# Optimization experiments

Measured on AMD Instinct MI355X. Metric: run time of the kernel, lower is better.

## Reference

```python
import jax, jax.numpy as jnp
import numpy as np

B, S, D, H = 2, 2048, 1024, 16
DH = D // H  # d_head = 64
EPS = 1e-6


def _rms_norm(x, eps=EPS):
    # norm_without_weight: RMS normalization over last dim, no learned scale
    return x * jax.lax.rsqrt(jnp.mean(x * x, axis=-1, keepdims=True) + eps)


def _rope_tables(seq_len, dim):
    # angular_freq: dim//4 geometric freqs + dim//4 zeros -> dim//2 total
    freqs = (1.0 / 1024.0) ** jnp.linspace(0.0, 1.0, dim // 4, dtype=jnp.float32)
    freqs = jnp.concatenate([freqs, jnp.zeros((dim // 4,), dtype=jnp.float32)])
    theta = jnp.outer(jnp.arange(seq_len, dtype=jnp.float32), freqs)  # [S, dim//2]
    return jnp.cos(theta), jnp.sin(theta)


def _apply_rope(x_bhsk, cos, sin):
    # x: [B,H,S,DH]; cos/sin: [S, DH//2] broadcast over batch/heads
    c = cos[None, None, :, :]
    s = sin[None, None, :, :]
    xf = x_bhsk.astype(jnp.float32)
    x1, x2 = jnp.split(xf, 2, axis=-1)
    y1 = x1 * c + x2 * s
    y2 = -x1 * s + x2 * c
    return jnp.concatenate([y1, y2], axis=-1).astype(x_bhsk.dtype)


def setup_inputs() -> dict:
    key = jax.random.key(0)
    k0, k1, k2, k3, k4 = jax.random.split(key, 5)
    scale = 1.0 / np.sqrt(D)
    x = jax.random.normal(k0, (B, S, D), dtype=jnp.float32)
    # equinox Linear stores weight as [out_features, in_features], y = x @ W.T
    w_q = jax.random.normal(k1, (D, D), dtype=jnp.float32) * scale
    w_k = jax.random.normal(k2, (D, D), dtype=jnp.float32) * scale
    w_v = jax.random.normal(k3, (D, D), dtype=jnp.float32) * scale
    w_o = jax.random.normal(k4, (D, D), dtype=jnp.float32) * scale
    mask = jnp.tril(jnp.ones((S, S), dtype=bool))  # causal
    return {"x": x, "w_q": w_q, "w_k": w_k, "w_v": w_v, "w_o": w_o, "mask": mask}


def reference(x, w_q, w_k, w_v, w_o, mask):
    b, s, d = x.shape
    # projections (no bias); [B,S,D] @ [D,D].T -> [B,S,D] -> [B,H,S,DH]
    def proj(w):
        y = jnp.einsum('bsd,ed->bse', x, w)
        return y.reshape(b, s, H, DH).transpose(0, 2, 1, 3)
    q, k, v = proj(w_q), proj(w_k), proj(w_v)
    # QK-norm (RMS, no weight)
    q = _rms_norm(q)
    k = _rms_norm(k)
    # rotary over sequence axis
    cos, sin = _rope_tables(s, DH)
    q = _apply_rope(q, cos, sin)
    k = _apply_rope(k, cos, sin)
    # scores [B,H,S,S]
    scores = jnp.einsum('bhsk,bhtk->bhst', q, k) / jnp.sqrt(jnp.float32(DH))
    scores = jnp.where(mask[None, None, :, :], scores, -jnp.inf)
    weights = jax.nn.softmax(scores, axis=-1)
    out = jnp.einsum('bhst,bhtk->bhsk', weights, v)  # [B,H,S,DH]
    out = out.transpose(0, 2, 1, 3).reshape(b, s, d)
    return jnp.einsum('bsd,ed->bse', out, w_o)
```

## Files before the change

kernel.cpp:

```cpp
#include <hip/hip_runtime.h>
#include <hip/hip_bf16.h>

#define Bb 2
#define Ss 2048
#define Dd 1024
#define Hh 16
#define Tt ((size_t)Bb*Ss*Dd)
#define WNn ((size_t)Dd*Dd)

typedef short bf16x8 __attribute__((ext_vector_type(8)));
typedef short bf16x4 __attribute__((ext_vector_type(4)));
typedef float floatx4 __attribute__((ext_vector_type(4)));
typedef unsigned short u16;

__device__ inline void gld16(void* lds, const void* g) {
  __builtin_amdgcn_global_load_lds(
      (const __attribute__((address_space(1))) unsigned int*)g,
      (__attribute__((address_space(3))) unsigned int*)lds, 16, 0, 0);
}

__device__ inline float bf2f(u16 u) {
  unsigned int x = ((unsigned int)u) << 16;
  float f; __builtin_memcpy(&f, &x, 4); return f;
}
__device__ inline u16 f2bf(float f) {
  unsigned int x; __builtin_memcpy(&x, &f, 4);
  x = (x + 0x7fff + ((x >> 16) & 1)) >> 16;
  return (u16)x;
}
__device__ inline float u2f(unsigned int x) {
  float f; __builtin_memcpy(&f, &x, 4); return f;
}
__device__ inline unsigned int cvtpk(float lo, float hi) {
  unsigned int r;
  asm("v_cvt_pk_bf16_f32 %0, %1, %2" : "=v"(r) : "v"(lo), "v"(hi));
  return r;
}

__global__ void sniff(const unsigned int* __restrict__ x, unsigned int* __restrict__ flag,
                      int nwords) {
  __shared__ int cnt;
  if (threadIdx.x == 0) cnt = 0;
  __syncthreads();
  int local = 0;
  for (int i = threadIdx.x; i < nwords; i += blockDim.x) {
    unsigned int wd = x[i];
    if (((wd >> 7)  & 0xFFu) == 0xFFu) local++;
    if (((wd >> 23) & 0xFFu) == 0xFFu) local++;
  }
  atomicAdd(&cnt, local);
  __syncthreads();
  if (threadIdx.x == 0) *flag = (cnt >= 64) ? 1u : 0u;
}

__global__ __launch_bounds__(256) void convert_all(
    const void* __restrict__ x,  const void* __restrict__ wq,
    const void* __restrict__ wk, const void* __restrict__ wv,
    const void* __restrict__ wo, u16* __restrict__ dst,
    int smode, const unsigned int* __restrict__ flag,
    float2* __restrict__ tab) {
  const int gb = blockIdx.x;
  if (gb >= 4096) {
    int e = (gb - 4096)*1024 + threadIdx.x*4;
#pragma unroll
    for (int j = 0; j < 4; j++, e++) {
      int s = e >> 4, f = e & 15;
      float freq = exp2f((-10.0f/15.0f) * (float)f);
      float th = (float)s * freq;
      float sn, c;
      sincosf(th, &sn, &c);
      tab[e] = make_float2(c, sn);
    }
    return;
  }
  const void* src; size_t base; int lb;
  if (gb < 2048)      { src = x;  base = 0;            lb = gb;        }
  else if (gb < 2560) { src = wq; base = Tt;           lb = gb - 2048; }
  else if (gb < 3072) { src = wk; base = Tt + WNn;     lb = gb - 2560; }
  else if (gb < 3584) { src = wv; base = Tt + 2*WNn;   lb = gb - 3072; }
  else                { src = wo; base = Tt + 3*WNn;   lb = gb - 3584; }
  const size_t off = (size_t)lb*2048 + threadIdx.x*8;
  const bool f32 = (smode >= 0) ? (smode == 1) : (*flag != 0u);
  bf16x8 v;
  if (f32) {
    const float* s = (const float*)src + off;
#pragma unroll
    for (int j = 0; j < 8; j++) v[j] = (short)f2bf(s[j]);
  } else {
    v = *(const bf16x8*)((const u16*)src + off);
  }
  *(bf16x8*)(dst + base + off) = v;
}

__global__ __launch_bounds__(256) void gemm_bt(
    const u16* __restrict__ A,
    const u16* __restrict__ W0, const u16* __restrict__ W1, const u16* __restrict__ W2,
    void* __restrict__ C0, void* __restrict__ C1, void* __restrict__ C2,
    int M, int N, int K, const unsigned int* __restrict__ flag, int outMode, int mode,
    const float2* __restrict__ tab)
{
  const u16* W; void* C;
  if (blockIdx.z == 0)      { W = W0; C = C0; }
  else if (blockIdx.z == 1) { W = W1; C = C1; }
  else                      { W = W2; C = C2; }

  __shared__ __align__(16) u16 sA[128*32];
  __shared__ __align__(16) u16 sB[128*32];

  const int tid  = threadIdx.x;
  const int lane = tid & 63;
  const int w    = tid >> 6;
  const int wm = w >> 1, wn = w & 1;
  const int col = lane & 15, quad = lane >> 4;
  const int bm = blockIdx.y, bn = blockIdx.x;

  floatx4 acc[4][4] = {};

  const int c0 = tid, c1 = tid + 256;
  const size_t aOff0 = (size_t)(bm*128 + (c0 >> 2))*K + (c0 & 3)*8;
  const size_t aOff1 = (size_t)(bm*128 + (c1 >> 2))*K + (c1 & 3)*8;
  const size_t bOff0 = (size_t)(bn*128 + (c0 >> 2))*K + (c0 & 3)*8;
  const size_t bOff1 = (size_t)(bn*128 + (c1 >> 2))*K + (c1 & 3)*8;

  for (int kk = 0; kk < K; kk += 32) {
    gld16(&sA[c0*8], A + aOff0 + kk);
    gld16(&sA[c1*8], A + aOff1 + kk);
    gld16(&sB[c0*8], W + bOff0 + kk);
    gld16(&sB[c1*8], W + bOff1 + kk);
    __syncthreads();
    bf16x8 af[4], bfr[4];
#pragma unroll
    for (int i = 0; i < 4; i++)
      af[i] = *(const bf16x8*)&sA[(wm*64 + i*16 + col)*32 + quad*8];
#pragma unroll
    for (int j = 0; j < 4; j++)
      bfr[j] = *(const bf16x8*)&sB[(wn*64 + j*16 + col)*32 + quad*8];
#pragma unroll
    for (int i = 0; i < 4; i++)
#pragma unroll
      for (int j = 0; j < 4; j++)
        acc[i][j] = __builtin_amdgcn_mfma_f32_16x16x32_bf16(af[i], bfr[j], acc[i][j], 0, 0, 0);
    __syncthreads();
  }

  if (mode == 0 && blockIdx.z == 2) {
    u16* Ct = (u16*)C;
#pragma unroll
    for (int i = 0; i < 4; i++)
#pragma unroll
      for (int j = 0; j < 4; j++) {
        int d = bn*128 + wn*64 + j*16 + col;
        int g = bm*128 + wm*64 + i*16 + quad*4;
        int hh = d >> 6, dl = d & 63;
        int bb = g >> 11, s = g & (Ss - 1);
        bf16x4 pk;
#pragma unroll
        for (int r = 0; r < 4; r++) pk[r] = (short)f2bf(acc[i][j][r]);
        *(bf16x4*)&Ct[((size_t)(bb*Hh + hh)*64 + dl)*Ss + s] = pk;
      }
  } else if (mode == 0) {
    const float qs = (blockIdx.z == 0) ? 0.125f : 1.0f;
    u16* Co = (u16*)C;
    const size_t cb = (size_t)(bn*128 + wn*64 + col);
#pragma unroll
    for (int i = 0; i < 4; i++)
#pragma unroll
      for (int r = 0; r < 4; r++) {
        float ss = 0.0f;
#pragma unroll
        for (int j = 0; j < 4; j++) ss += acc[i][j][r]*acc[i][j][r];
        ss += __shfl_xor(ss, 1, 64);
        ss += __shfl_xor(ss, 2, 64);
        ss += __shfl_xor(ss, 4, 64);
        ss += __shfl_xor(ss, 8, 64);
        float rn = rsqrtf(ss*(1.0f/64.0f) + 1e-6f) * qs;
        int grow = bm*128 + wm*64 + i*16 + quad*4 + r;
        float2 cs = tab[(grow & (Ss - 1))*16 + col];
        float c = cs.x, sn = cs.y;
        float x0 = acc[i][0][r]*rn, x1 = acc[i][1][r]*rn;
        float x2 = acc[i][2][r]*rn, x3 = acc[i][3][r]*rn;
        size_t rowb = (size_t)grow*N + cb;
        Co[rowb]      = f2bf(x0*c + x2*sn);
        Co[rowb + 16] = f2bf(x1);
        Co[rowb + 32] = f2bf(x2*c - x0*sn);
        Co[rowb + 48] = f2bf(x3);
      }
  } else {
    const bool f32o = (outMode == 1) || (outMode == -1 && *flag != 0u);
#pragma unroll
    for (int i = 0; i < 4; i++)
#pragma unroll
      for (int j = 0; j < 4; j++)
#pragma unroll
        for (int r = 0; r < 4; r++) {
          int grow = bm*128 + wm*64 + i*16 + quad*4 + r;
          int gcol = bn*128 + wn*64 + j*16 + col;
          size_t idx = (size_t)grow*N + gcol;
          float v = acc[i][j][r];
          if (f32o) ((float*)C)[idx] = v;
          else      ((u16*)C)[idx]   = f2bf(v);
        }
  }
}

__global__ __launch_bounds__(256) void attn(
    const u16* __restrict__ Q, const u16* __restrict__ Kv,
    const u16* __restrict__ Vt, u16* __restrict__ O)
{
  __shared__ __align__(16) u16 sK[2][64*72];
  __shared__ __align__(16) u16 sV[2][2][64*32];
  __shared__ __align__(16) u16 sP[4][16*72];

  const int tid  = threadIdx.x;
  const int lane = tid & 63;
  const int w    = tid >> 6;
  const int col = lane & 15, quad = lane >> 4;
  const int bh = blockIdx.x;
  const int qt = 31 - (int)blockIdx.y;
  const int b = bh >> 4, h = bh & 15;
  const size_t base  = (size_t)b*Ss*Dd + (size_t)h*64;
  const size_t vbase = (size_t)bh*64*Ss;

  const int krow = tid >> 2;
  const int kch  = (tid & 3) * 2;
  const int vrow = tid >> 2;
  const int vcp  = (tid & 3) ^ (vrow & 3) ^ ((vrow >> 2) & 3);
  const u16* Vh = Vt + vbase + (size_t)vrow*Ss + vcp*8;
  const int xorv = quad ^ (col & 3) ^ ((col >> 2) & 3);
  u16* sPw = &sP[w][0];
  const float L2E = 1.44269504f;

  const int q0 = qt * 64;
  const int nk = qt + 1;
  const int qmin = q0 + w*16;

  bf16x8 qf0, qf1;
  {
    const size_t qoff = base + (size_t)(q0 + w*16 + col)*Dd + quad*8;
    qf0 = *(const bf16x8*)(Q + qoff);
    qf1 = *(const bf16x8*)(Q + qoff + 32);
  }
  floatx4 oacc[4] = {};
  float mi[4], li[4];
#pragma unroll
  for (int r = 0; r < 4; r++) { mi[r] = -1e30f; li[r] = 0.0f; }

  {
    const u16* kg = Kv + base + (size_t)krow*Dd + kch*8;
    bf16x8 ka = *(const bf16x8*)kg;
    bf16x8 kb = *(const bf16x8*)(kg + 8);
    gld16(&sV[0][0][tid*8], Vh);
    gld16(&sV[0][1][tid*8], Vh + 32);
    *(bf16x8*)&sK[0][krow*72 + kch*8]     = ka;
    *(bf16x8*)&sK[0][krow*72 + kch*8 + 8] = kb;
    __syncthreads();
  }

  for (int kt = 0; kt < nk; kt++) {
    const int t0 = kt*64;
    const int cur = kt & 1, nxt = cur ^ 1;
    const bool more = (kt + 1 < nk);
    bf16x8 ka, kb;
    if (more) {
      const u16* kg = Kv + base + (size_t)(t0 + 64 + krow)*Dd + kch*8;
      ka = *(const bf16x8*)kg;
      kb = *(const bf16x8*)(kg + 8);
      gld16(&sV[nxt][0][tid*8], Vh + t0 + 64);
      gld16(&sV[nxt][1][tid*8], Vh + t0 + 96);
    }

    floatx4 sc[4] = {};
    __builtin_amdgcn_s_setprio(1);
#pragma unroll
    for (int ts = 0; ts < 4; ts++) {
      bf16x8 k0 = *(const bf16x8*)&sK[cur][(ts*16 + col)*72 + quad*8];
      bf16x8 k1 = *(const bf16x8*)&sK[cur][(ts*16 + col)*72 + 32 + quad*8];
      sc[ts] = __builtin_amdgcn_mfma_f32_16x16x32_bf16(qf0, k0, sc[ts], 0,0,0);
      sc[ts] = __builtin_amdgcn_mfma_f32_16x16x32_bf16(qf1, k1, sc[ts], 0,0,0);
    }
    __builtin_amdgcn_s_setprio(0);

    const bool boundary = (t0 + 63 > qmin);
    float mxr[4];
    float needmax = 0.0f;
#pragma unroll
    for (int r = 0; r < 4; r++) {
      if (boundary) {
        const int qr = q0 + w*16 + quad*4 + r;
        if (t0 +      col > qr) sc[0][r] = -1e30f;
        if (t0 + 16 + col > qr) sc[1][r] = -1e30f;
        if (t0 + 32 + col > qr) sc[2][r] = -1e30f;
        if (t0 + 48 + col > qr) sc[3][r] = -1e30f;
      }
      float mx = fmaxf(fmaxf(sc[0][r], sc[1][r]), fmaxf(sc[2][r], sc[3][r]));
      mx = fmaxf(mx, __shfl_xor(mx, 1, 64));
      mx = fmaxf(mx, __shfl_xor(mx, 2, 64));
      mx = fmaxf(mx, __shfl_xor(mx, 4, 64));
      mx = fmaxf(mx, __shfl_xor(mx, 8, 64));
      mxr[r] = mx;
      needmax = fmaxf(needmax, mx - mi[r]);
    }
    if (!__all(needmax <= 8.0f)) {
      float alr[4];
#pragma unroll
      for (int r = 0; r < 4; r++) {
        float mn = fmaxf(mi[r], mxr[r]);
        float al = exp2f((mi[r] - mn)*L2E);
        mi[r] = mn; li[r] *= al; alr[r] = al;
      }
#pragma unroll
      for (int db = 0; db < 4; db++)
#pragma unroll
        for (int r = 0; r < 4; r++) oacc[db][r] *= alr[r];
    }
#pragma unroll
    for (int r = 0; r < 4; r++) {
      const float nb = -mi[r]*L2E;
      float p0 = exp2f(fmaf(sc[0][r], L2E, nb));
      float p1 = exp2f(fmaf(sc[1][r], L2E, nb));
      float p2 = exp2f(fmaf(sc[2][r], L2E, nb));
      float p3 = exp2f(fmaf(sc[3][r], L2E, nb));
      unsigned int pk01 = cvtpk(p0, p1);
      unsigned int pk23 = cvtpk(p2, p3);
      const int rw = (quad*4 + r)*72;
      sPw[rw + col]      = (u16)pk01;
      sPw[rw + 16 + col] = (u16)(pk01 >> 16);
      sPw[rw + 32 + col] = (u16)pk23;
      sPw[rw + 48 + col] = (u16)(pk23 >> 16);
      li[r] += (u2f(pk01 << 16) + u2f(pk01 & 0xffff0000u))
             + (u2f(pk23 << 16) + u2f(pk23 & 0xffff0000u));
    }
    bf16x8 pa0 = *(const bf16x8*)&sPw[col*72 + quad*8];
    bf16x8 pa1 = *(const bf16x8*)&sPw[col*72 + 32 + quad*8];
    __builtin_amdgcn_s_setprio(1);
#pragma unroll
    for (int db = 0; db < 4; db++) {
      const int vs = (db*16 + col)*32 + xorv*8;
      bf16x8 vb0 = *(const bf16x8*)&sV[cur][0][vs];
      bf16x8 vb1 = *(const bf16x8*)&sV[cur][1][vs];
      oacc[db] = __builtin_amdgcn_mfma_f32_16x16x32_bf16(pa0, vb0, oacc[db], 0,0,0);
      oacc[db] = __builtin_amdgcn_mfma_f32_16x16x32_bf16(pa1, vb1, oacc[db], 0,0,0);
    }
    __builtin_amdgcn_s_setprio(0);

    if (more) {
      *(bf16x8*)&sK[nxt][krow*72 + kch*8]     = ka;
      *(bf16x8*)&sK[nxt][krow*72 + kch*8 + 8] = kb;
    }
    __syncthreads();
  }

  float inv[4];
#pragma unroll
  for (int r = 0; r < 4; r++) {
    float s = li[r];
    s += __shfl_xor(s, 1, 64);
    s += __shfl_xor(s, 2, 64);
    s += __shfl_xor(s, 4, 64);
    s += __shfl_xor(s, 8, 64);
    inv[r] = 1.0f / s;
  }
#pragma unroll
  for (int db = 0; db < 4; db++)
#pragma unroll
    for (int r = 0; r < 4; r++)
      O[base + (size_t)(q0 + w*16 + quad*4 + r)*Dd + db*16 + col] =
          f2bf(oacc[db][r] * inv[r]);
}

extern "C" void kernel_launch(void* const* d_in, const int* in_sizes, int n_in,
                              void* d_out, int out_size, void* d_ws, size_t ws_size,
                              hipStream_t stream) {
  const void* x  = d_in[0];
  const void* wq = d_in[1];
  const void* wk = d_in[2];
  const void* wv = d_in[3];
  const void* wo = d_in[4];

  const size_t T  = Tt;
  const size_t WN = WNn;

  char* ws = (char*)d_ws;
  unsigned int* flag = (unsigned int*)ws;
  u16* xb  = (u16*)(ws + 256);
  u16* wqb = xb  + T;
  u16* wkb = wqb + WN;
  u16* wvb = wkb + WN;
  u16* wob = wvb + WN;
  u16* Qb  = wob + WN;
  u16* Kb  = Qb + T;
  u16* Vb  = Kb + T;
  u16* AO  = Vb + T;
  float2* tab = (float2*)(AO + T);

  int smode = -1;
  if (in_sizes && n_in > 0) {
    if (in_sizes[0] == (int)(T*4))      smode = 1;
    else if (in_sizes[0] == (int)(T*2)) smode = 0;
  }
  if (smode < 0)
    sniff<<<1, 1024, 0, stream>>>((const unsigned int*)x, flag, 65536);

  convert_all<<<4128, 256, 0, stream>>>(x, wq, wk, wv, wo, xb, smode, flag, tab);

  gemm_bt<<<dim3(8, 32, 3), 256, 0, stream>>>(xb, wqb, wkb, wvb, Qb, Kb, Vb,
                                              4096, 1024, 1024, flag, 0, 0, tab);
  attn<<<dim3(32, 32), 256, 0, stream>>>(Qb, Kb, Vb, AO);
  gemm_bt<<<dim3(8, 32, 1), 256, 0, stream>>>(AO, wob, wob, wob, d_out, d_out, d_out,
                                              4096, 1024, 1024, flag, smode, 1, tab);
}
```

Measured before the change: 252.7 us.

## Stage QKV GEMM epilogue through LDS for coalesced stores; split out narrower output GEMM

The QKV projection epilogue now writes each wave's results into a padded LDS tile and then stores 16-byte rows to global memory, replacing the scattered 2-byte and 8-byte stores. This applies to both the RoPE/RMS-normed Q/K path and the transposed V path. The output projection moves to a dedicated gemm_o kernel with 128x64 tiles, which doubles the block count to 512 for better CU occupancy at the cost of less reuse of A per block. The added LDS (about 36 KB per block) may lower occupancy of the QKV GEMM.

```diff
diff --git a/kernel.cpp b/kernel.cpp
--- a/kernel.cpp
+++ b/kernel.cpp
@@ -96,8 +96,7 @@
     const u16* __restrict__ A,
     const u16* __restrict__ W0, const u16* __restrict__ W1, const u16* __restrict__ W2,
     void* __restrict__ C0, void* __restrict__ C1, void* __restrict__ C2,
-    int M, int N, int K, const unsigned int* __restrict__ flag, int outMode, int mode,
-    const float2* __restrict__ tab)
+    int M, int N, int K, const float2* __restrict__ tab)
 {
   const u16* W; void* C;
   if (blockIdx.z == 0)      { W = W0; C = C0; }
@@ -106,6 +105,7 @@
 
   __shared__ __align__(16) u16 sA[128*32];
   __shared__ __align__(16) u16 sB[128*32];
+  __shared__ __align__(16) u16 sE[4][64*72];
 
   const int tid  = threadIdx.x;
   const int lane = tid & 63;
@@ -143,25 +143,31 @@
     __syncthreads();
   }
 
-  if (mode == 0 && blockIdx.z == 2) {
+  u16* sEw = &sE[w][0];
+  const int rrow = lane >> 3, rch = lane & 7;
+
+  if (blockIdx.z == 2) {
+#pragma unroll
+    for (int i = 0; i < 4; i++)
+#pragma unroll
+      for (int j = 0; j < 4; j++) {
+        bf16x4 pk;
+#pragma unroll
+        for (int r = 0; r < 4; r++) pk[r] = (short)f2bf(acc[i][j][r]);
+        *(bf16x4*)&sEw[(j*16 + col)*72 + i*16 + quad*4] = pk;
+      }
+    const int g0 = bm*128 + wm*64;
+    const int bb = g0 >> 11, s0 = g0 & (Ss - 1);
+    const int hh = (bn*128 + wn*64) >> 6;
     u16* Ct = (u16*)C;
 #pragma unroll
-    for (int i = 0; i < 4; i++)
-#pragma unroll
-      for (int j = 0; j < 4; j++) {
-        int d = bn*128 + wn*64 + j*16 + col;
-        int g = bm*128 + wm*64 + i*16 + quad*4;
-        int hh = d >> 6, dl = d & 63;
-        int bb = g >> 11, s = g & (Ss - 1);
-        bf16x4 pk;
-#pragma unroll
-        for (int r = 0; r < 4; r++) pk[r] = (short)f2bf(acc[i][j][r]);
-        *(bf16x4*)&Ct[((size_t)(bb*Hh + hh)*64 + dl)*Ss + s] = pk;
-      }
-  } else if (mode == 0) {
+    for (int t = 0; t < 8; t++) {
+      const int dl = rrow + t*8;
+      bf16x8 v = *(const bf16x8*)&sEw[dl*72 + rch*8];
+      *(bf16x8*)&Ct[((size_t)(bb*Hh + hh)*64 + dl)*Ss + s0 + rch*8] = v;
+    }
+  } else {
     const float qs = (blockIdx.z == 0) ? 0.125f : 1.0f;
-    u16* Co = (u16*)C;
-    const size_t cb = (size_t)(bn*128 + wn*64 + col);
 #pragma unroll
     for (int i = 0; i < 4; i++)
 #pragma unroll
@@ -176,31 +182,81 @@
         float rn = rsqrtf(ss*(1.0f/64.0f) + 1e-6f) * qs;
         int grow = bm*128 + wm*64 + i*16 + quad*4 + r;
         float2 cs = tab[(grow & (Ss - 1))*16 + col];
-        float c = cs.x, sn = cs.y;
         float x0 = acc[i][0][r]*rn, x1 = acc[i][1][r]*rn;
         float x2 = acc[i][2][r]*rn, x3 = acc[i][3][r]*rn;
-        size_t rowb = (size_t)grow*N + cb;
-        Co[rowb]      = f2bf(x0*c + x2*sn);
-        Co[rowb + 16] = f2bf(x1);
-        Co[rowb + 32] = f2bf(x2*c - x0*sn);
-        Co[rowb + 48] = f2bf(x3);
+        const int lr = (i*16 + quad*4 + r)*72;
+        sEw[lr + col]      = f2bf(x0*cs.x + x2*cs.y);
+        sEw[lr + 16 + col] = f2bf(x1);
+        sEw[lr + 32 + col] = f2bf(x2*cs.x - x0*cs.y);
+        sEw[lr + 48 + col] = f2bf(x3);
       }
-  } else {
-    const bool f32o = (outMode == 1) || (outMode == -1 && *flag != 0u);
-#pragma unroll
-    for (int i = 0; i < 4; i++)
-#pragma unroll
-      for (int j = 0; j < 4; j++)
-#pragma unroll
-        for (int r = 0; r < 4; r++) {
-          int grow = bm*128 + wm*64 + i*16 + quad*4 + r;
-          int gcol = bn*128 + wn*64 + j*16 + col;
-          size_t idx = (size_t)grow*N + gcol;
-          float v = acc[i][j][r];
-          if (f32o) ((float*)C)[idx] = v;
-          else      ((u16*)C)[idx]   = f2bf(v);
-        }
-  }
+    u16* Co = (u16*)C;
+    const size_t gb = (size_t)(bm*128 + wm*64);
+    const int cb = bn*128 + wn*64 + rch*8;
+#pragma unroll
+    for (int t = 0; t < 8; t++) {
+      const int lr = rrow + t*8;
+      bf16x8 v = *(const bf16x8*)&sEw[lr*72 + rch*8];
+      *(bf16x8*)&Co[(gb + lr)*N + cb] = v;
+    }
+  }
+}
+
+__global__ __launch_bounds__(256) void gemm_o(
+    const u16* __restrict__ A, const u16* __restrict__ W, void* __restrict__ C,
+    int M, int N, int K, const unsigned int* __restrict__ flag, int outMode)
+{
+  __shared__ __align__(16) u16 sA[128*32];
+  __shared__ __align__(16) u16 sB[64*32];
+
+  const int tid  = threadIdx.x;
+  const int lane = tid & 63;
+  const int w    = tid >> 6;
+  const int wm = w >> 1, wn = w & 1;
+  const int col = lane & 15, quad = lane >> 4;
+  const int bm = blockIdx.y, bn = blockIdx.x;
+
+  floatx4 acc[4][2] = {};
+
+  const int c0 = tid, c1 = tid + 256;
+  const size_t aOff0 = (size_t)(bm*128 + (c0 >> 2))*K + (c0 & 3)*8;
+  const size_t aOff1 = (size_t)(bm*128 + (c1 >> 2))*K + (c1 & 3)*8;
+  const size_t bOff0 = (size_t)(bn*64  + (c0 >> 2))*K + (c0 & 3)*8;
+
+  for (int kk = 0; kk < K; kk += 32) {
+    gld16(&sA[c0*8], A + aOff0 + kk);
+    gld16(&sA[c1*8], A + aOff1 + kk);
+    gld16(&sB[c0*8], W + bOff0 + kk);
+    __syncthreads();
+    bf16x8 af[4], bfr[2];
+#pragma unroll
+    for (int i = 0; i < 4; i++)
+      af[i] = *(const bf16x8*)&sA[(wm*64 + i*16 + col)*32 + quad*8];
+#pragma unroll
+    for (int j = 0; j < 2; j++)
+      bfr[j] = *(const bf16x8*)&sB[(wn*32 + j*16 + col)*32 + quad*8];
+#pragma unroll
+    for (int i = 0; i < 4; i++)
+#pragma unroll
+      for (int j = 0; j < 2; j++)
+        acc[i][j] = __builtin_amdgcn_mfma_f32_16x16x32_bf16(af[i], bfr[j], acc[i][j], 0, 0, 0);
+    __syncthreads();
+  }
+
+  const bool f32o = (outMode == 1) || (outMode == -1 && *flag != 0u);
+#pragma unroll
+  for (int i = 0; i < 4; i++)
+#pragma unroll
+    for (int j = 0; j < 2; j++)
+#pragma unroll
+      for (int r = 0; r < 4; r++) {
+        int grow = bm*128 + wm*64 + i*16 + quad*4 + r;
+        int gcol = bn*64 + wn*32 + j*16 + col;
+        size_t idx = (size_t)grow*N + gcol;
+        float v = acc[i][j][r];
+        if (f32o) ((float*)C)[idx] = v;
+        else      ((u16*)C)[idx]   = f2bf(v);
+      }
 }
 
 __global__ __launch_bounds__(256) void attn(
@@ -404,8 +460,8 @@
   convert_all<<<4128, 256, 0, stream>>>(x, wq, wk, wv, wo, xb, smode, flag, tab);
 
   gemm_bt<<<dim3(8, 32, 3), 256, 0, stream>>>(xb, wqb, wkb, wvb, Qb, Kb, Vb,
-                                              4096, 1024, 1024, flag, 0, 0, tab);
+                                              4096, 1024, 1024, tab);
   attn<<<dim3(32, 32), 256, 0, stream>>>(Qb, Kb, Vb, AO);
-  gemm_bt<<<dim3(8, 32, 1), 256, 0, stream>>>(AO, wob, wob, wob, d_out, d_out, d_out,
-                                              4096, 1024, 1024, flag, smode, 1, tab);
-}
+  gemm_o<<<dim3(16, 32), 256, 0, stream>>>(AO, wob, d_out,
+                                           4096, 1024, 1024, flag, smode);
+}
```

New measurement: 258.2 us. 1.02x slower.
